# Kernel tuning notes

Hardware: AMD Instinct MI355X
Metric: run time of the kernel (lower is better)

Reference implementation:

```python
import jax, jax.numpy as jnp
import numpy as np

B, U, HEADS, S = 16, 1024, 8, 1024


def setup_inputs() -> dict:
    key = jax.random.key(0)
    k1, k2, k3, k4 = jax.random.split(key, 4)
    x = jax.random.normal(k1, (B, U, S), dtype=jnp.float32)
    mask = jax.random.randint(k2, (B, S, S), 0, 2).astype(bool)
    w_qkv = jax.random.normal(k3, (3 * U, U), dtype=jnp.float32) * 0.02
    w_out = jax.random.normal(k4, (U, U), dtype=jnp.float32) * 0.02
    return {"x": x, "mask": mask, "w_qkv": w_qkv, "w_out": w_out}


def reference(x, mask, w_qkv, w_out):
    # x: (B, U, S), mask: (B, n_queries, n_keys) bool
    b, u, s = x.shape
    h = HEADS
    c = u // h  # head (chunk) size
    scale = 1.0 / np.sqrt(c).astype(np.float32)

    # 1x1-conv QKV projection (bias=False): (3U, U) x (B, U, S) -> (B, 3U, S)
    qkv = jnp.einsum('ou,bus->bos', w_qkv, x)
    Q, K, V = jnp.split(qkv, 3, axis=1)           # each (B, U, S)
    Qh = Q.reshape(b, h, c, s)
    Kh = K.reshape(b, h, c, s)
    Vh = V.reshape(b, h, c, s)

    # attention logits: (B, H, n_q, n_k)
    A = jnp.einsum('bhcq,bhck->bhqk', Qh, Kh)

    # relu activation with per-query valid-key-count normalization
    m = mask.sum(axis=2)[:, :, None]              # (B, n_q, 1) count of valid keys
    n_elem = jnp.where(mask, m, 1).astype(A.dtype)[:, None]  # (B, 1, n_q, n_k)
    mask_b = mask[:, None]                        # broadcast over heads
    A = jnp.where(mask_b, jax.nn.relu(A) * scale, -jnp.inf)
    A = A / n_elem
    A = jnp.where(jnp.isinf(A), jnp.zeros((), A.dtype), A)

    # attention-value aggregation (faithful math of broadcast+sum): (B, H, C, n_q)
    Ch = jnp.einsum('bhqk,bhck->bhcq', A, Vh)
    Cc = Ch.reshape(b, u, s)

    # finishing 1x1-conv linear layer
    return jnp.einsum('ou,bus->bos', w_out, Cc)
```

## Files before the change

### kernel.cpp

```cpp
#include <hip/hip_runtime.h>

#define B_DIM 16
#define U_DIM 1024
#define H_DIM 8
#define S_DIM 1024
#define C_DIM 128
#define KD 1024
#define SCALE 0.08838834764831845f

typedef __attribute__((ext_vector_type(8))) short s16x8;
typedef __attribute__((ext_vector_type(4))) float f32x4;

__device__ __forceinline__ void gll16(const void* g, void* l) {
  __builtin_amdgcn_global_load_lds(
      (const __attribute__((address_space(1))) unsigned int*)g,
      (__attribute__((address_space(3))) unsigned int*)l, 16, 0, 0);
}
__device__ __forceinline__ unsigned short f2bf(float f) {
  unsigned u = __float_as_uint(f);
  u += 0x7FFF + ((u >> 16) & 1u);
  return (unsigned short)(u >> 16);
}
#define MFMA16(a, b, c) __builtin_amdgcn_mfma_f32_16x16x32_bf16(a, b, c, 0, 0, 0)

__global__ void detect_mask(const unsigned char* __restrict__ mask_raw, int* __restrict__ flag) {
  __shared__ int not01, notf;
  if (threadIdx.x == 0) { not01 = 0; notf = 0; }
  __syncthreads();
  const unsigned int* p = (const unsigned int*)mask_raw;
  int l01 = 0, lf = 0;
  for (int i = threadIdx.x; i < 4096; i += 256) {
    unsigned int v = p[i];
    if (v != 0u && v != 1u) l01 = 1;
    if (v != 0u && v != 0x3F800000u) lf = 1;
  }
  if (l01) atomicOr(&not01, 1);
  if (lf) atomicOr(&notf, 1);
  __syncthreads();
  if (threadIdx.x == 0) flag[0] = (!not01) ? 0 : ((!notf) ? 2 : 1);
}

__global__ __launch_bounds__(256) void pack_mask(const unsigned char* __restrict__ mask_raw,
                                                 const int* __restrict__ flag,
                                                 unsigned long long* __restrict__ bits) {
  __shared__ unsigned char tile[64][80];
  const int t = threadIdx.x;
  const int kt = blockIdx.x * 64, qw = blockIdx.y, b = blockIdx.z;
  const int mk = flag[0];
  const int q = t >> 2, kbase = (t & 3) * 16;
  const size_t row = (size_t)(b * S_DIM + qw * 64 + q);
  if (mk == 1) {
    uint4 v = *(const uint4*)(mask_raw + (row << 10) + kt + kbase);
    *(uint4*)&tile[q][kbase] = v;
  } else if (mk == 0) {
    const int* p = (const int*)mask_raw + (row << 10) + kt + kbase;
#pragma unroll
    for (int j = 0; j < 4; ++j) {
      int4 v = ((const int4*)p)[j];
      uchar4 o;
      o.x = v.x ? 1 : 0; o.y = v.y ? 1 : 0; o.z = v.z ? 1 : 0; o.w = v.w ? 1 : 0;
      *(uchar4*)&tile[q][kbase + j * 4] = o;
    }
  } else {
    const float* p = (const float*)mask_raw + (row << 10) + kt + kbase;
#pragma unroll
    for (int j = 0; j < 4; ++j) {
      float4 v = ((const float4*)p)[j];
      uchar4 o;
      o.x = (v.x != 0.f) ? 1 : 0; o.y = (v.y != 0.f) ? 1 : 0;
      o.z = (v.z != 0.f) ? 1 : 0; o.w = (v.w != 0.f) ? 1 : 0;
      *(uchar4*)&tile[q][kbase + j * 4] = o;
    }
  }
  __syncthreads();
  const int wave = t >> 6, lane = t & 63;
#pragma unroll
  for (int qq = 0; qq < 16; ++qq) {
    int qr = wave * 16 + qq;
    unsigned long long bal = __ballot(tile[qr][lane] != 0);
    if (lane == 0)
      bits[(size_t)blockIdx.x * (B_DIM * S_DIM) + (size_t)b * S_DIM + qw * 64 + qr] = bal;
  }
}

__global__ __launch_bounds__(256) void invm_from_bits(const unsigned long long* __restrict__ bits,
                                                      float* __restrict__ invm) {
  int idx = blockIdx.x * 256 + threadIdx.x;
  int s = 0;
#pragma unroll
  for (int kt = 0; kt < S_DIM / 64; ++kt)
    s += __popcll(bits[(size_t)kt * (B_DIM * S_DIM) + idx]);
  invm[idx] = (s > 0) ? (SCALE / (float)s) : 0.f;
}

__global__ __launch_bounds__(256) void cvt_bf16(const float* __restrict__ in,
                                                unsigned short* __restrict__ out, int n) {
  int i = (blockIdx.x * 256 + threadIdx.x) * 4;
  if (i < n) {
    float4 v = *(const float4*)(in + i);
    ushort4 o;
    o.x = f2bf(v.x); o.y = f2bf(v.y); o.z = f2bf(v.z); o.w = f2bf(v.w);
    *(ushort4*)(out + i) = o;
  }
}

__global__ __launch_bounds__(256) void transpose_x(const float* __restrict__ x,
                                                   unsigned short* __restrict__ xT) {
  __shared__ float T[32][33];
  const int t = threadIdx.x, r = t >> 3, c4 = (t & 7) * 4;
  const int s0 = blockIdx.x * 32, u0 = blockIdx.y * 32;
  const size_t base = (size_t)blockIdx.z * U_DIM * S_DIM;
  float4 v = *(const float4*)(x + base + (size_t)(u0 + r) * S_DIM + s0 + c4);
  T[r][c4 + 0] = v.x; T[r][c4 + 1] = v.y; T[r][c4 + 2] = v.z; T[r][c4 + 3] = v.w;
  __syncthreads();
  ushort4 o;
  o.x = f2bf(T[c4 + 0][r]); o.y = f2bf(T[c4 + 1][r]);
  o.z = f2bf(T[c4 + 2][r]); o.w = f2bf(T[c4 + 3][r]);
  *(ushort4*)(xT + base + (size_t)(s0 + r) * U_DIM + u0 + c4) = o;
}

__global__ __launch_bounds__(256) void transpose_v(const unsigned short* __restrict__ qkvT,
                                                   unsigned short* __restrict__ VT) {
  __shared__ unsigned short T[32][34];
  const int t = threadIdx.x, r = t >> 3, c4 = (t & 7) * 4;
  const int k0 = blockIdx.x * 32, c0 = blockIdx.y * 32;
  const unsigned short* qb = qkvT + (size_t)blockIdx.z * S_DIM * (3 * U_DIM);
  ushort4 v = *(const ushort4*)(qb + (size_t)(k0 + r) * (3 * U_DIM) + 2 * U_DIM + c0 + c4);
  T[r][c4 + 0] = v.x; T[r][c4 + 1] = v.y; T[r][c4 + 2] = v.z; T[r][c4 + 3] = v.w;
  __syncthreads();
  ushort4 o;
  o.x = T[c4 + 0][r]; o.y = T[c4 + 1][r]; o.z = T[c4 + 2][r]; o.w = T[c4 + 3][r];
  *(ushort4*)(VT + (size_t)blockIdx.z * U_DIM * S_DIM + (size_t)(c0 + r) * S_DIM + k0 + c4) = o;
}

template <typename OUT>
__global__ __launch_bounds__(512, 2) void gemm256(const unsigned short* __restrict__ A,
                                                  const unsigned short* __restrict__ Bm,
                                                  OUT* __restrict__ D,
                                                  long long sAb, long long sBb, long long sDb,
                                                  int N) {
  __shared__ unsigned short sA0[256 * 64], sB0[256 * 64];
  __shared__ unsigned short sA1[256 * 64], sB1[256 * 64];
  const int tid = threadIdx.x;
  const int wave = tid >> 6, lane = tid & 63;
  const int l15 = lane & 15, quad = lane >> 4;
  const int wm = wave & 3, wn = wave >> 2;
  const unsigned int Lb = blockIdx.x + gridDim.x * (blockIdx.y + gridDim.y * blockIdx.z);
  const unsigned int nwg = gridDim.x * gridDim.y * gridDim.z;
  const unsigned int logical = (Lb & 7u) * (nwg >> 3) + (Lb >> 3);
  const int bx = logical % gridDim.x;
  const unsigned int rem = logical / gridDim.x;
  const int by = rem % gridDim.y;
  const int bz = rem / gridDim.y;
  const int m0 = by * 256, n0 = bx * 256;
  A += (size_t)bz * sAb + (size_t)m0 * KD;
  Bm += (size_t)bz * sBb + (size_t)n0 * KD;
  D += (size_t)bz * sDb;

  const int r0 = tid >> 3;
  const int kc0 = (tid & 7) ^ (r0 & 7);
  const unsigned short* pA = A + (size_t)r0 * KD + kc0 * 8;
  const unsigned short* pB = Bm + (size_t)r0 * KD + kc0 * 8;
  const int wo = wave * 512;

#define STG_U0(SA, K0)                                        \
  do {                                                        \
    gll16(pA + (K0), &(SA)[wo]);                              \
    gll16(pA + 64 * KD + (K0), &(SA)[4096 + wo]);             \
  } while (0)
#define STG_U1(SA, K0)                                        \
  do {                                                        \
    gll16(pA + 128 * KD + (K0), &(SA)[8192 + wo]);            \
    gll16(pA + 192 * KD + (K0), &(SA)[12288 + wo]);           \
  } while (0)
#define STG_U2(SB, K0)                                        \
  do {                                                        \
    gll16(pB + (K0), &(SB)[wo]);                              \
    gll16(pB + 128 * KD + (K0), &(SB)[8192 + wo]);            \
  } while (0)
#define STG_U3(SB, K0)                                        \
  do {                                                        \
    gll16(pB + 64 * KD + (K0), &(SB)[4096 + wo]);             \
    gll16(pB + 192 * KD + (K0), &(SB)[12288 + wo]);           \
  } while (0)

#define WAITB(VN)                                             \
  do {                                                        \
    asm volatile("s_waitcnt vmcnt(" #VN ")" ::: "memory");    \
    __builtin_amdgcn_s_barrier();                             \
    asm volatile("" ::: "memory");                            \
  } while (0)

  s16x8 a[4][2];
  f32x4 acc[4][8] = {};

#define LDA(SA)                                                                         \
  do {                                                                                  \
    _Pragma("unroll") for (int i = 0; i < 4; ++i) {                                     \
      int row = wm * 64 + i * 16 + l15;                                                 \
      _Pragma("unroll") for (int ks = 0; ks < 2; ++ks)                                  \
          a[i][ks] = *(const s16x8*)&(SA)[row * 64 + (((ks * 4 + quad) ^ (row & 7)) * 8)]; \
    }                                                                                   \
  } while (0)

#define PHASE(SB, P)                                                                    \
  do {                                                                                  \
    s16x8 b[2][2];                                                                      \
    _Pragma("unroll") for (int jj = 0; jj < 2; ++jj) {                                  \
      int row = wn * 128 + ((P) * 2 + jj) * 16 + l15;                                   \
      _Pragma("unroll") for (int ks = 0; ks < 2; ++ks)                                  \
          b[jj][ks] = *(const s16x8*)&(SB)[row * 64 + (((ks * 4 + quad) ^ (row & 7)) * 8)]; \
    }                                                                                   \
    __builtin_amdgcn_s_setprio(1);                                                      \
    _Pragma("unroll") for (int ks = 0; ks < 2; ++ks)                                    \
        _Pragma("unroll") for (int i = 0; i < 4; ++i)                                   \
            _Pragma("unroll") for (int jj = 0; jj < 2; ++jj)                            \
                acc[i][(P) * 2 + jj] = MFMA16(a[i][ks], b[jj][ks], acc[i][(P) * 2 + jj]); \
    __builtin_amdgcn_s_setprio(0);                                                      \
  } while (0)

#define TILE(SA, SB, SAn, SBn, K1)                            \
  do {                                                        \
    WAITB(2);                                                 \
    STG_U0(SAn, K1);                                          \
    LDA(SA);                                                  \
    PHASE(SB, 0);                                             \
    STG_U1(SAn, K1);                                          \
    PHASE(SB, 1);                                             \
    WAITB(4);                                                 \
    STG_U2(SBn, K1);                                          \
    PHASE(SB, 2);                                             \
    STG_U3(SBn, K1);                                          \
    PHASE(SB, 3);                                             \
  } while (0)

#define TILE_LAST(CA, CB)                                     \
  do {                                                        \
    WAITB(2);                                                 \
    LDA(CA);                                                  \
    PHASE(CB, 0);                                             \
    PHASE(CB, 1);                                             \
    WAITB(0);                                                 \
    PHASE(CB, 2);                                             \
    PHASE(CB, 3);                                             \
  } while (0)

  STG_U0(sA0, 0); STG_U1(sA0, 0); STG_U2(sB0, 0); STG_U3(sB0, 0);

  for (int kt = 0; kt < 14; kt += 2) {
    TILE(sA0, sB0, sA1, sB1, (kt + 1) * 64);
    TILE(sA1, sB1, sA0, sB0, (kt + 2) * 64);
  }
  TILE(sA0, sB0, sA1, sB1, 15 * 64);
  TILE_LAST(sA1, sB1);
#undef TILE
#undef TILE_LAST
#undef PHASE
#undef LDA
#undef WAITB
#undef STG_U0
#undef STG_U1
#undef STG_U2
#undef STG_U3

#pragma unroll
  for (int i = 0; i < 4; ++i)
#pragma unroll
    for (int j = 0; j < 8; ++j) {
      f32x4 v = acc[i][j];
#pragma unroll
      for (int r = 0; r < 4; ++r) {
        int m = m0 + wm * 64 + i * 16 + quad * 4 + r;
        int n = n0 + wn * 128 + j * 16 + l15;
        if constexpr (sizeof(OUT) == 2) D[(size_t)m * N + n] = f2bf(v[r]);
        else D[(size_t)m * N + n] = v[r];
      }
    }
}

__global__ __launch_bounds__(1024, 4) void attn_mfma(const unsigned short* __restrict__ qkvT,
                                                     const unsigned short* __restrict__ VT,
                                                     const unsigned long long* __restrict__ bits,
                                                     const float* __restrict__ invm,
                                                     unsigned short* __restrict__ CcT, int b0) {
  __shared__ unsigned short QV[64 * 128];
  __shared__ unsigned short Ks0[64 * 128];
  __shared__ unsigned short Ks1[64 * 128];
  __shared__ unsigned short Vs[128 * 64];
  __shared__ unsigned short Ps[128 * 64];

  const int tid = threadIdx.x, wave = tid >> 6, lane = tid & 63;
  const int l15 = lane & 15, quad = lane >> 4;
  const int qq = wave >> 2, kw = wave & 3;
  const int L = blockIdx.x + 8 * (blockIdx.y + 8 * blockIdx.z);
  const int cpx = (8 * H_DIM * gridDim.z) >> 3;
  const int logical = (L & 7) * cpx + (L >> 3);
  const int qt = logical & 7, h = (logical >> 3) & 7, z = logical >> 6;
  const int q0 = qt * 128, b = b0 + z;
  const unsigned short* qB = qkvT + (size_t)z * S_DIM * (3 * U_DIM);
  const unsigned short* Vb = VT + (size_t)z * U_DIM * S_DIM + (size_t)h * C_DIM * S_DIM;

  const int srow = tid >> 4, sc = (tid & 15) ^ (srow & 7);
  const int vrow = tid >> 3, vkc = (tid & 7) ^ (vrow & 7);

  gll16(qB + (size_t)(q0 + srow) * (3 * U_DIM) + h * C_DIM + sc * 8, &QV[tid * 8]);
  gll16(qB + (size_t)srow * (3 * U_DIM) + U_DIM + h * C_DIM + sc * 8, &Ks0[tid * 8]);
  gll16(Vb + (size_t)vrow * S_DIM + vkc * 8, &Vs[tid * 8]);
  __syncthreads();

  s16x8 qf[2][4];
  if (qq < 2) {
#pragma unroll
    for (int j = 0; j < 2; ++j)
#pragma unroll
      for (int kk = 0; kk < 4; ++kk) {
        int row = qq * 32 + j * 16 + l15;
        qf[j][kk] = *(const s16x8*)&QV[row * 128 + ((kk * 4 + quad) ^ (row & 7)) * 8];
      }
  }
  __syncthreads();

  gll16(qB + (size_t)(q0 + 64 + srow) * (3 * U_DIM) + h * C_DIM + sc * 8, &QV[tid * 8]);
  __syncthreads();

  if (qq >= 2) {
#pragma unroll
    for (int j = 0; j < 2; ++j)
#pragma unroll
      for (int kk = 0; kk < 4; ++kk) {
        int row = (qq - 2) * 32 + j * 16 + l15;
        qf[j][kk] = *(const s16x8*)&QV[row * 128 + ((kk * 4 + quad) ^ (row & 7)) * 8];
      }
  }
  float invf[2];
  {
    const float* ivp = invm + (size_t)b * S_DIM + q0 + qq * 32;
#pragma unroll
    for (int j = 0; j < 2; ++j) invf[j] = ivp[j * 16 + l15];
  }
  __syncthreads();

  f32x4 pacc[2][2] = {};

  for (int kt = 0; kt < S_DIM / 64; ++kt) {
    const unsigned short* kcur = (kt & 1) ? Ks1 : Ks0;
    unsigned short* knxt = (kt & 1) ? Ks0 : Ks1;
    const unsigned short* vcur = (kt & 1) ? QV : Vs;
    unsigned short* vnxt = (kt & 1) ? Vs : QV;

    if (kt < S_DIM / 64 - 1) {
      const int kn = (kt + 1) * 64;
      gll16(qB + (size_t)(kn + srow) * (3 * U_DIM) + U_DIM + h * C_DIM + sc * 8,
            &knxt[tid * 8]);
      gll16(Vb + (size_t)vrow * S_DIM + kn + vkc * 8, &vnxt[tid * 8]);
    }

    unsigned long long w64[2];
    {
      const unsigned long long* mw =
          bits + (size_t)kt * (B_DIM * S_DIM) + (size_t)b * S_DIM + q0 + qq * 32;
#pragma unroll
      for (int j = 0; j < 2; ++j) w64[j] = mw[j * 16 + l15];
    }

    s16x8 af[4];
#pragma unroll
    for (int kk = 0; kk < 4; ++kk) {
      int row = kw * 16 + l15;
      af[kk] = *(const s16x8*)&kcur[row * 128 + ((kk * 4 + quad) ^ (row & 7)) * 8];
    }
    f32x4 sacc[2] = {};
    __builtin_amdgcn_s_setprio(1);
#pragma unroll
    for (int kk = 0; kk < 4; ++kk)
#pragma unroll
      for (int j = 0; j < 2; ++j) sacc[j] = MFMA16(af[kk], qf[j][kk], sacc[j]);
    __builtin_amdgcn_s_setprio(0);

#pragma unroll
    for (int j = 0; j < 2; ++j) {
      const unsigned int m4 = (unsigned int)(w64[j] >> (kw * 16 + quad * 4)) & 0xFu;
      float p[4];
#pragma unroll
      for (int r = 0; r < 4; ++r) {
        float t = fmaxf(sacc[j][r], 0.f) * invf[j];
        p[r] = ((m4 >> r) & 1u) ? t : 0.f;
      }
      unsigned int pk0, pk1;
      asm("v_cvt_pk_bf16_f32 %0, %1, %2" : "=v"(pk0) : "v"(p[0]), "v"(p[1]));
      asm("v_cvt_pk_bf16_f32 %0, %1, %2" : "=v"(pk1) : "v"(p[2]), "v"(p[3]));
      int q = qq * 32 + j * 16 + l15;
      int chunk = (kw * 2 + (quad >> 1)) ^ (q & 7);
      *(uint2*)&Ps[q * 64 + chunk * 8 + (quad & 1) * 4] = make_uint2(pk0, pk1);
    }

    asm volatile("s_waitcnt lgkmcnt(0)" ::: "memory");
    __builtin_amdgcn_sched_barrier(0);
    __builtin_amdgcn_s_barrier();
    __builtin_amdgcn_sched_barrier(0);

#pragma unroll
    for (int ks = 0; ks < 2; ++ks) {
      s16x8 pf[2], vf[2];
#pragma unroll
      for (int i = 0; i < 2; ++i) {
        int row = qq * 32 + i * 16 + l15;
        pf[i] = *(const s16x8*)&Ps[row * 64 + ((ks * 4 + quad) ^ (row & 7)) * 8];
      }
#pragma unroll
      for (int j = 0; j < 2; ++j) {
        int row = kw * 32 + j * 16 + l15;
        vf[j] = *(const s16x8*)&vcur[row * 64 + ((ks * 4 + quad) ^ (row & 7)) * 8];
      }
      __builtin_amdgcn_s_setprio(1);
#pragma unroll
      for (int i = 0; i < 2; ++i)
#pragma unroll
        for (int j = 0; j < 2; ++j) pacc[i][j] = MFMA16(pf[i], vf[j], pacc[i][j]);
      __builtin_amdgcn_s_setprio(0);
    }
    __syncthreads();
  }

  unsigned short* cb = CcT + (size_t)z * S_DIM * U_DIM;
#pragma unroll
  for (int i = 0; i < 2; ++i)
#pragma unroll
    for (int j = 0; j < 2; ++j) {
      f32x4 v = pacc[i][j];
#pragma unroll
      for (int r = 0; r < 4; ++r) {
        int q = q0 + qq * 32 + i * 16 + quad * 4 + r;
        int c = h * C_DIM + kw * 32 + j * 16 + l15;
        cb[(size_t)q * U_DIM + c] = f2bf(v[r]);
      }
    }
}

extern "C" void kernel_launch(void* const* d_in, const int* in_sizes, int n_in,
                              void* d_out, int out_size, void* d_ws, size_t ws_size,
                              hipStream_t stream) {
  const float* x = (const float*)d_in[0];
  const unsigned char* mask_raw = (const unsigned char*)d_in[1];
  const float* w_qkv = (const float*)d_in[2];
  const float* w_out = (const float*)d_in[3];
  float* out = (float*)d_out;

  char* ws = (char*)d_ws;
  int* flag = (int*)ws;
  float* invm = (float*)(ws + 256);
  unsigned long long* bits = (unsigned long long*)(ws + 256 + 65536);
  unsigned short* wqkv_bf = (unsigned short*)((char*)bits + (size_t)B_DIM * S_DIM * 16 * 8);
  unsigned short* wout_bf = (unsigned short*)((char*)wqkv_bf + (size_t)3 * U_DIM * U_DIM * 2);
  char* heap = (char*)wout_bf + (size_t)U_DIM * U_DIM * 2;

  const size_t xT_pb = (size_t)U_DIM * S_DIM * 2;
  const size_t qkvT_pb = (size_t)3 * U_DIM * S_DIM * 2;
  const size_t vT_pb = (size_t)U_DIM * S_DIM * 2;
  const size_t ccT_pb = (size_t)U_DIM * S_DIM * 2;
  const size_t per_batch = xT_pb + qkvT_pb + vT_pb + ccT_pb;
  const size_t fixed = (size_t)(heap - ws);
  int nb = (ws_size > fixed) ? (int)((ws_size - fixed) / per_batch) : 1;
  if (nb < 1) nb = 1;
  if (nb > B_DIM) nb = B_DIM;

  unsigned short* xT = (unsigned short*)heap;
  unsigned short* qkvT = (unsigned short*)(heap + (size_t)nb * xT_pb);
  unsigned short* VT = (unsigned short*)(heap + (size_t)nb * (xT_pb + qkvT_pb));
  unsigned short* CcT = (unsigned short*)(heap + (size_t)nb * (xT_pb + qkvT_pb + vT_pb));

  detect_mask<<<1, 256, 0, stream>>>(mask_raw, flag);
  pack_mask<<<dim3(S_DIM / 64, S_DIM / 64, B_DIM), 256, 0, stream>>>(mask_raw, flag, bits);
  invm_from_bits<<<(B_DIM * S_DIM) / 256, 256, 0, stream>>>(bits, invm);
  cvt_bf16<<<(3 * U_DIM * U_DIM) / 1024, 256, 0, stream>>>(w_qkv, wqkv_bf, 3 * U_DIM * U_DIM);
  cvt_bf16<<<(U_DIM * U_DIM) / 1024, 256, 0, stream>>>(w_out, wout_bf, U_DIM * U_DIM);

  for (int b0 = 0; b0 < B_DIM; b0 += nb) {
    int cnt = (B_DIM - b0 < nb) ? (B_DIM - b0) : nb;
    transpose_x<<<dim3(S_DIM / 32, U_DIM / 32, cnt), 256, 0, stream>>>(
        x + (size_t)b0 * U_DIM * S_DIM, xT);
    gemm256<unsigned short><<<dim3(3 * U_DIM / 256, S_DIM / 256, cnt), 512, 0, stream>>>(
        xT, wqkv_bf, qkvT, (long long)U_DIM * S_DIM, 0LL, (long long)3 * U_DIM * S_DIM, 3 * U_DIM);
    transpose_v<<<dim3(S_DIM / 32, U_DIM / 32, cnt), 256, 0, stream>>>(qkvT, VT);
    attn_mfma<<<dim3(S_DIM / 128, H_DIM, cnt), 1024, 0, stream>>>(
        qkvT, VT, bits, invm, CcT, b0);
    gemm256<float><<<dim3(S_DIM / 256, U_DIM / 256, cnt), 512, 0, stream>>>(
        wout_bf, CcT, out + (size_t)b0 * U_DIM * S_DIM, 0LL,
        (long long)U_DIM * S_DIM, (long long)U_DIM * S_DIM, S_DIM);
  }
}
```

Before: 445.0 us.

## Restructure GEMM main loop into stutter-barrier phases separating LDS reads from MFMA

Splits each phase into an LDS read step for B fragments and an MFMA step. Each step is bracketed by workgroup barriers so that waves alternate between memory and compute in lockstep. The vmcnt waits are moved so that global-to-LDS prefetches for the next tile are issued earlier and waited on at finer granularity. The goal is to overlap LDS traffic and MFMA across waves and keep the matrix cores busy, at the cost of many more barriers per tile.

```diff
diff --git a/kernel.cpp b/kernel.cpp
--- a/kernel.cpp
+++ b/kernel.cpp
@@ -184,14 +184,16 @@
     gll16(pB + 192 * KD + (K0), &(SB)[12288 + wo]);           \
   } while (0)
 
-#define WAITB(VN)                                             \
-  do {                                                        \
-    asm volatile("s_waitcnt vmcnt(" #VN ")" ::: "memory");    \
+#define BARR()                                                \
+  do {                                                        \
+    asm volatile("" ::: "memory");                            \
     __builtin_amdgcn_s_barrier();                             \
     asm volatile("" ::: "memory");                            \
   } while (0)
+#define VMC(NN) asm volatile("s_waitcnt vmcnt(" #NN ")" ::: "memory")
 
   s16x8 a[4][2];
+  s16x8 b[2][2];
   f32x4 acc[4][8] = {};
 
 #define LDA(SA)                                                                         \
@@ -203,14 +205,17 @@
     }                                                                                   \
   } while (0)
 
-#define PHASE(SB, P)                                                                    \
+#define DSRB(SB, P)                                                                     \
   do {                                                                                  \
-    s16x8 b[2][2];                                                                      \
     _Pragma("unroll") for (int jj = 0; jj < 2; ++jj) {                                  \
       int row = wn * 128 + ((P) * 2 + jj) * 16 + l15;                                   \
       _Pragma("unroll") for (int ks = 0; ks < 2; ++ks)                                  \
           b[jj][ks] = *(const s16x8*)&(SB)[row * 64 + (((ks * 4 + quad) ^ (row & 7)) * 8)]; \
     }                                                                                   \
+  } while (0)
+
+#define MM(P)                                                                           \
+  do {                                                                                  \
     __builtin_amdgcn_s_setprio(1);                                                      \
     _Pragma("unroll") for (int ks = 0; ks < 2; ++ks)                                    \
         _Pragma("unroll") for (int i = 0; i < 4; ++i)                                   \
@@ -219,45 +224,45 @@
     __builtin_amdgcn_s_setprio(0);                                                      \
   } while (0)
 
-#define TILE(SA, SB, SAn, SBn, K1)                            \
-  do {                                                        \
-    WAITB(2);                                                 \
-    STG_U0(SAn, K1);                                          \
-    LDA(SA);                                                  \
-    PHASE(SB, 0);                                             \
-    STG_U1(SAn, K1);                                          \
-    PHASE(SB, 1);                                             \
-    WAITB(4);                                                 \
-    STG_U2(SBn, K1);                                          \
-    PHASE(SB, 2);                                             \
-    STG_U3(SBn, K1);                                          \
-    PHASE(SB, 3);                                             \
+#define TILE_ST(CA, CB, NA, NB, K1)                           \
+  do {                                                        \
+    STG_U0(NA, K1);                                           \
+    STG_U1(NA, K1);                                           \
+    LDA(CA);                                                  \
+    DSRB(CB, 0); BARR(); MM(0); BARR();                       \
+    STG_U2(NB, K1);                                           \
+    DSRB(CB, 1); VMC(6); BARR(); MM(1); BARR();               \
+    STG_U3(NB, K1);                                           \
+    DSRB(CB, 2); BARR(); MM(2); BARR();                       \
+    DSRB(CB, 3); VMC(2); BARR(); MM(3); BARR();               \
   } while (0)
 
 #define TILE_LAST(CA, CB)                                     \
   do {                                                        \
-    WAITB(2);                                                 \
     LDA(CA);                                                  \
-    PHASE(CB, 0);                                             \
-    PHASE(CB, 1);                                             \
-    WAITB(0);                                                 \
-    PHASE(CB, 2);                                             \
-    PHASE(CB, 3);                                             \
+    DSRB(CB, 0); BARR(); MM(0); BARR();                       \
+    DSRB(CB, 1); VMC(0); BARR(); MM(1); BARR();               \
+    DSRB(CB, 2); BARR(); MM(2); BARR();                       \
+    DSRB(CB, 3); MM(3);                                       \
   } while (0)
 
   STG_U0(sA0, 0); STG_U1(sA0, 0); STG_U2(sB0, 0); STG_U3(sB0, 0);
+  VMC(2);
+  BARR();
 
   for (int kt = 0; kt < 14; kt += 2) {
-    TILE(sA0, sB0, sA1, sB1, (kt + 1) * 64);
-    TILE(sA1, sB1, sA0, sB0, (kt + 2) * 64);
-  }
-  TILE(sA0, sB0, sA1, sB1, 15 * 64);
+    TILE_ST(sA0, sB0, sA1, sB1, (kt + 1) * 64);
+    TILE_ST(sA1, sB1, sA0, sB0, (kt + 2) * 64);
+  }
+  TILE_ST(sA0, sB0, sA1, sB1, 15 * 64);
   TILE_LAST(sA1, sB1);
-#undef TILE
+#undef TILE_ST
 #undef TILE_LAST
-#undef PHASE
+#undef MM
+#undef DSRB
 #undef LDA
-#undef WAITB
+#undef VMC
+#undef BARR
 #undef STG_U0
 #undef STG_U1
 #undef STG_U2
```

After: 461.5 us. 3.7% more time.
